# Performance work log

Hardware: AMD Instinct MI355X
Metric: run time of the kernel (lower is better)

The kernel has to match this reference:

```python
import jax, jax.numpy as jnp
import numpy as np

N_NODES = 50000
N_EDGES = 800000
D = 64
N_BASIS = 8


def setup_inputs() -> dict:
    key = jax.random.key(0)
    ks = jax.random.split(key, 16)
    inp = {
        "p": jax.random.normal(ks[0], (N_NODES, D), dtype=jnp.float32),
        "idx_i": jax.random.randint(ks[1], (N_EDGES,), 0, N_NODES),
        "idx_j": jax.random.randint(ks[2], (N_EDGES,), 0, N_NODES),
        "basis": jax.random.normal(ks[3], (N_EDGES, N_BASIS), dtype=jnp.float32),
        # pp_layer MLP: [64, 64, 64], activation tanh between layers
        "pp_W1": jax.random.normal(ks[4], (D, D), dtype=jnp.float32) / np.sqrt(D),
        "pp_b1": jnp.zeros((D,), dtype=jnp.float32),
        "pp_W2": jax.random.normal(ks[5], (D, D), dtype=jnp.float32) / np.sqrt(D),
        "pp_b2": jnp.zeros((D,), dtype=jnp.float32),
        # pi_layer MLP: n_neurons = [128, 64, 64, 64*8], activation=None, last layer no bias
        "pi_W1": jax.random.normal(ks[6], (2 * D, D), dtype=jnp.float32) / np.sqrt(2 * D),
        "pi_b1": jnp.zeros((D,), dtype=jnp.float32),
        "pi_W2": jax.random.normal(ks[7], (D, D), dtype=jnp.float32) / np.sqrt(D),
        "pi_b2": jnp.zeros((D,), dtype=jnp.float32),
        "pi_W3": jax.random.normal(ks[8], (D, D * N_BASIS), dtype=jnp.float32) / np.sqrt(D),
        # ii_layer MLP: [64, 64, 64], activation tanh between layers
        "ii_W1": jax.random.normal(ks[9], (D, D), dtype=jnp.float32) / np.sqrt(D),
        "ii_b1": jnp.zeros((D,), dtype=jnp.float32),
        "ii_W2": jax.random.normal(ks[10], (D, D), dtype=jnp.float32) / np.sqrt(D),
        "ii_b2": jnp.zeros((D,), dtype=jnp.float32),
    }
    return inp


def reference(p, idx_i, idx_j, basis,
              pp_W1, pp_b1, pp_W2, pp_b2,
              pi_W1, pi_b1, pi_W2, pi_b2, pi_W3,
              ii_W1, ii_b1, ii_W2, ii_b2):
    # pp_layer: node MLP (tanh between layers, no activation after last)
    p1 = jnp.tanh(p @ pp_W1 + pp_b1) @ pp_W2 + pp_b2          # [N, D]

    # PILayer: gather endpoint features, concat, linear MLP (activation=None), basis contraction
    inter = jnp.concatenate([p1[idx_i], p1[idx_j]], axis=-1)  # [E, 2D]
    inter = inter @ pi_W1 + pi_b1                              # [E, D]
    inter = inter @ pi_W2 + pi_b2                              # [E, D]
    inter = inter @ pi_W3                                      # [E, D*n_basis] (no bias)
    inter = inter.reshape(inter.shape[0], D, N_BASIS)          # [E, D, n_basis]
    i1 = jnp.einsum('ecb,eb->ec', inter, basis)                # [E, D]

    # ii_layer: edge MLP
    i1 = jnp.tanh(i1 @ ii_W1 + ii_b1) @ ii_W2 + ii_b2          # [E, D]

    # IPLayer: scatter_add edge features back to nodes (dim_size = p1.shape[0])
    out = jax.ops.segment_sum(i1, idx_j, num_segments=p1.shape[0])  # [N, D]
    return out
```

## Files before the change

kernel.cpp:

```cpp
#include <hip/hip_runtime.h>

#define N_NODES 50000
#define N_EDGES 800000

typedef float f32x4 __attribute__((ext_vector_type(4)));
typedef short bf16x8 __attribute__((ext_vector_type(8)));

__device__ __forceinline__ float fast_tanh(float x) {
  float e = __expf(2.0f * x);
  return 1.0f - 2.0f / (e + 1.0f);
}

__device__ __forceinline__ unsigned short f2bf_rne(float x) {
  unsigned u = __float_as_uint(x);
  unsigned r = u + 0x7FFFu + ((u >> 16) & 1u);
  return (unsigned short)(r >> 16);
}

__global__ __launch_bounds__(256) void prep1_kernel(
    const float* __restrict__ piW1, const float* __restrict__ pib1,
    const float* __restrict__ piW2, const float* __restrict__ pib2,
    float* __restrict__ W12, float* __restrict__ b12) {
  int gid = blockIdx.x * 256 + threadIdx.x;
  if (gid < 128 * 64) {
    int m = gid >> 6, c = gid & 63;
    float acc = 0.f;
    #pragma unroll 8
    for (int k = 0; k < 64; ++k) acc = fmaf(piW1[m * 64 + k], piW2[k * 64 + c], acc);
    W12[gid] = acc;
  } else if (gid < 128 * 64 + 64) {
    int c = gid - 128 * 64;
    float acc = pib2[c];
    for (int k = 0; k < 64; ++k) acc = fmaf(pib1[k], piW2[k * 64 + c], acc);
    b12[c] = acc;
  }
}

__global__ __launch_bounds__(256) void prep_b_kernel(
    const float* __restrict__ piW3, const float* __restrict__ iiW1,
    unsigned short* __restrict__ Bpack) {
  int gid = blockIdx.x * 256 + threadIdx.x;
  int j = gid & 7;
  int lane = (gid >> 3) & 63;
  int ct = (gid >> 9) & 3;
  int ks = gid >> 11;
  int kidx = ks * 32 + ((lane >> 4) << 3) + j;
  int col = ct * 16 + (lane & 15);
  int k = kidx >> 3, b = kidx & 7;
  float acc = 0.f;
  #pragma unroll 8
  for (int mm = 0; mm < 64; ++mm)
    acc = fmaf(piW3[k * 512 + mm * 8 + b], iiW1[mm * 64 + col], acc);
  Bpack[gid] = f2bf_rne(acc);
}

__global__ __launch_bounds__(256) void prep_w2_kernel(
    const float* __restrict__ iiW2, unsigned short* __restrict__ W2pack) {
  int gid = blockIdx.x * 256 + threadIdx.x;
  int j = gid & 7;
  int lane = (gid >> 3) & 63;
  int ct = (gid >> 9) & 3;
  int ks = gid >> 11;
  int kidx = ks * 32 + ((lane >> 4) << 3) + j;
  int col = ct * 16 + (lane & 15);
  W2pack[gid] = f2bf_rne(iiW2[kidx * 64 + col]);
}

__global__ __launch_bounds__(256) void node_kernel(
    const float* __restrict__ p,
    const float* __restrict__ ppW1, const float* __restrict__ ppb1,
    const float* __restrict__ ppW2, const float* __restrict__ ppb2,
    const float* __restrict__ W12,
    float* __restrict__ qa, float* __restrict__ qb) {
  __shared__ float sW1[64 * 64];
  __shared__ float sW2[64 * 64];
  __shared__ float sW12[128 * 64];
  __shared__ float sb1[64], sb2[64];
  __shared__ float sX[4][8][64];
  int tid = threadIdx.x;
  for (int i = tid; i < 64 * 64; i += 256) { sW1[i] = ppW1[i]; sW2[i] = ppW2[i]; }
  for (int i = tid; i < 128 * 64; i += 256) sW12[i] = W12[i];
  if (tid < 64) { sb1[tid] = ppb1[tid]; sb2[tid] = ppb2[tid]; }
  __syncthreads();
  int wave = tid >> 6, lane = tid & 63;
  int rowbase = blockIdx.x * 32 + wave * 8;

  float4* sXf4 = (float4*)&sX[wave][0][0];
  for (int t = lane; t < 128; t += 64) {
    int r = t >> 4, c4 = t & 15;
    int row = rowbase + r;
    float4 v = make_float4(0.f, 0.f, 0.f, 0.f);
    if (row < N_NODES) v = ((const float4*)p)[row * 16 + c4];
    sXf4[t] = v;
  }
  __syncthreads();

  float h[8];
  #pragma unroll
  for (int r = 0; r < 8; ++r) h[r] = sb1[lane];
  for (int k = 0; k < 64; ++k) {
    float w = sW1[k * 64 + lane];
    #pragma unroll
    for (int r = 0; r < 8; ++r) h[r] = fmaf(sX[wave][r][k], w, h[r]);
  }
  #pragma unroll
  for (int r = 0; r < 8; ++r) h[r] = fast_tanh(h[r]);
  __syncthreads();
  #pragma unroll
  for (int r = 0; r < 8; ++r) sX[wave][r][lane] = h[r];
  __syncthreads();

  float g[8];
  #pragma unroll
  for (int r = 0; r < 8; ++r) g[r] = sb2[lane];
  for (int k = 0; k < 64; ++k) {
    float w = sW2[k * 64 + lane];
    #pragma unroll
    for (int r = 0; r < 8; ++r) g[r] = fmaf(sX[wave][r][k], w, g[r]);
  }
  __syncthreads();
  #pragma unroll
  for (int r = 0; r < 8; ++r) sX[wave][r][lane] = g[r];
  __syncthreads();

  float a[8], b[8];
  #pragma unroll
  for (int r = 0; r < 8; ++r) { a[r] = 0.f; b[r] = 0.f; }
  for (int k = 0; k < 64; ++k) {
    float wa = sW12[k * 64 + lane];
    float wb = sW12[(64 + k) * 64 + lane];
    #pragma unroll
    for (int r = 0; r < 8; ++r) {
      float x = sX[wave][r][k];
      a[r] = fmaf(x, wa, a[r]);
      b[r] = fmaf(x, wb, b[r]);
    }
  }
  #pragma unroll
  for (int r = 0; r < 8; ++r) {
    int row = rowbase + r;
    if (row < N_NODES) {
      qa[row * 64 + lane] = a[r];
      qb[row * 64 + lane] = b[r];
    }
  }
}

__global__ __launch_bounds__(512, 4) void edge_kernel(
    const int* __restrict__ idx_i, const int* __restrict__ idx_j,
    const float* __restrict__ basis,
    const float* __restrict__ qa, const float* __restrict__ qb,
    const float* __restrict__ b12,
    const unsigned short* __restrict__ Bpack,
    const unsigned short* __restrict__ W2pack,
    const float* __restrict__ iib1, const float* __restrict__ iib2,
    float* __restrict__ out) {
  __shared__ __align__(16) unsigned short sB[32768];
  float* sH2 = (float*)sB;
  unsigned short* sT = sB;

  int tid = threadIdx.x;
  int e0 = blockIdx.x * 128;

  for (int t = tid; t < 2048; t += 512) {
    int e = t >> 4, q = t & 15;
    int ii = idx_i[e0 + e];
    int jj = idx_j[e0 + e];
    float4 va = ((const float4*)qa)[ii * 16 + q];
    float4 vb = ((const float4*)qb)[jj * 16 + q];
    float4 vc = ((const float4*)b12)[q];
    float4 h;
    h.x = va.x + vb.x + vc.x;
    h.y = va.y + vb.y + vc.y;
    h.z = va.z + vb.z + vc.z;
    h.w = va.w + vb.w + vc.w;
    ((float4*)(sH2 + e * 68))[q] = h;
  }
  __syncthreads();

  int w = tid >> 6, l = tid & 63;
  int m = l & 15, s = l >> 4;
  int eloc = w * 16 + m;

  float h2r[16];
  #pragma unroll
  for (int t = 0; t < 16; ++t) h2r[t] = sH2[eloc * 68 + t * 4 + s];

  float bas[8];
  {
    const float4* bp = (const float4*)(basis + (size_t)(e0 + eloc) * 8);
    float4 b0 = bp[0], b1 = bp[1];
    bas[0] = b0.x; bas[1] = b0.y; bas[2] = b0.z; bas[3] = b0.w;
    bas[4] = b1.x; bas[5] = b1.y; bas[6] = b1.z; bas[7] = b1.w;
  }
  __syncthreads();

  {
    const uint4* g = (const uint4*)Bpack;
    uint4* d = (uint4*)sB;
    #pragma unroll
    for (int t = 0; t < 8; ++t) d[tid + t * 512] = g[tid + t * 512];
  }
  __syncthreads();

  f32x4 c0, c1, c2, c3;
  {
    float v0 = iib1[m], v1 = iib1[16 + m], v2 = iib1[32 + m], v3 = iib1[48 + m];
    c0 = (f32x4){v0, v0, v0, v0};
    c1 = (f32x4){v1, v1, v1, v1};
    c2 = (f32x4){v2, v2, v2, v2};
    c3 = (f32x4){v3, v3, v3, v3};
  }

  const bf16x8* Bl = (const bf16x8*)sB;
  #pragma unroll
  for (int ks = 0; ks < 16; ++ks) {
    bf16x8 B0 = Bl[(ks * 4 + 0) * 64 + l];
    bf16x8 B1 = Bl[(ks * 4 + 1) * 64 + l];
    bf16x8 B2 = Bl[(ks * 4 + 2) * 64 + l];
    bf16x8 B3 = Bl[(ks * 4 + 3) * 64 + l];
    float hv = h2r[ks];
    union { unsigned u[4]; bf16x8 v; } Ah, Al;
    #pragma unroll
    for (int jj2 = 0; jj2 < 4; ++jj2) {
      float p0 = hv * bas[2 * jj2];
      float p1 = hv * bas[2 * jj2 + 1];
      unsigned u0 = __float_as_uint(p0), u1 = __float_as_uint(p1);
      unsigned h0 = u0 & 0xFFFF0000u, h1 = u1 & 0xFFFF0000u;
      Ah.u[jj2] = (u0 >> 16) | h1;
      float l0 = p0 - __uint_as_float(h0);
      float l1 = p1 - __uint_as_float(h1);
      Al.u[jj2] = (__float_as_uint(l0) >> 16) | (__float_as_uint(l1) & 0xFFFF0000u);
    }
    c0 = __builtin_amdgcn_mfma_f32_16x16x32_bf16(Ah.v, B0, c0, 0, 0, 0);
    c1 = __builtin_amdgcn_mfma_f32_16x16x32_bf16(Ah.v, B1, c1, 0, 0, 0);
    c2 = __builtin_amdgcn_mfma_f32_16x16x32_bf16(Ah.v, B2, c2, 0, 0, 0);
    c3 = __builtin_amdgcn_mfma_f32_16x16x32_bf16(Ah.v, B3, c3, 0, 0, 0);
    c0 = __builtin_amdgcn_mfma_f32_16x16x32_bf16(Al.v, B0, c0, 0, 0, 0);
    c1 = __builtin_amdgcn_mfma_f32_16x16x32_bf16(Al.v, B1, c1, 0, 0, 0);
    c2 = __builtin_amdgcn_mfma_f32_16x16x32_bf16(Al.v, B2, c2, 0, 0, 0);
    c3 = __builtin_amdgcn_mfma_f32_16x16x32_bf16(Al.v, B3, c3, 0, 0, 0);
  }
  __syncthreads();

  #pragma unroll
  for (int r = 0; r < 4; ++r) {
    int row = w * 16 + s * 4 + r;
    sT[row * 72 + 0 * 16 + m] = f2bf_rne(fast_tanh(c0[r]));
    sT[row * 72 + 1 * 16 + m] = f2bf_rne(fast_tanh(c1[r]));
    sT[row * 72 + 2 * 16 + m] = f2bf_rne(fast_tanh(c2[r]));
    sT[row * 72 + 3 * 16 + m] = f2bf_rne(fast_tanh(c3[r]));
  }
  __syncthreads();

  f32x4 d0, d1, d2, d3;
  {
    float v0 = iib2[m], v1 = iib2[16 + m], v2 = iib2[32 + m], v3 = iib2[48 + m];
    d0 = (f32x4){v0, v0, v0, v0};
    d1 = (f32x4){v1, v1, v1, v1};
    d2 = (f32x4){v2, v2, v2, v2};
    d3 = (f32x4){v3, v3, v3, v3};
  }
  const bf16x8* Wl = (const bf16x8*)W2pack;
  #pragma unroll
  for (int ks = 0; ks < 2; ++ks) {
    bf16x8 Af = *(const bf16x8*)(sT + eloc * 72 + ks * 32 + s * 8);
    d0 = __builtin_amdgcn_mfma_f32_16x16x32_bf16(Af, Wl[(ks * 4 + 0) * 64 + l], d0, 0, 0, 0);
    d1 = __builtin_amdgcn_mfma_f32_16x16x32_bf16(Af, Wl[(ks * 4 + 1) * 64 + l], d1, 0, 0, 0);
    d2 = __builtin_amdgcn_mfma_f32_16x16x32_bf16(Af, Wl[(ks * 4 + 2) * 64 + l], d2, 0, 0, 0);
    d3 = __builtin_amdgcn_mfma_f32_16x16x32_bf16(Af, Wl[(ks * 4 + 3) * 64 + l], d3, 0, 0, 0);
  }

  #pragma unroll
  for (int r = 0; r < 4; ++r) {
    int jj = idx_j[e0 + w * 16 + s * 4 + r];
    float* po = out + (size_t)jj * 64;
    atomicAdd(po + m, d0[r]);
    atomicAdd(po + 16 + m, d1[r]);
    atomicAdd(po + 32 + m, d2[r]);
    atomicAdd(po + 48 + m, d3[r]);
  }
}

extern "C" void kernel_launch(void* const* d_in, const int* in_sizes, int n_in,
                              void* d_out, int out_size, void* d_ws, size_t ws_size,
                              hipStream_t stream) {
  const float* p     = (const float*)d_in[0];
  const int*   idx_i = (const int*)d_in[1];
  const int*   idx_j = (const int*)d_in[2];
  const float* basis = (const float*)d_in[3];
  const float* ppW1  = (const float*)d_in[4];
  const float* ppb1  = (const float*)d_in[5];
  const float* ppW2  = (const float*)d_in[6];
  const float* ppb2  = (const float*)d_in[7];
  const float* piW1  = (const float*)d_in[8];
  const float* pib1  = (const float*)d_in[9];
  const float* piW2  = (const float*)d_in[10];
  const float* pib2  = (const float*)d_in[11];
  const float* piW3  = (const float*)d_in[12];
  const float* iiW1  = (const float*)d_in[13];
  const float* iib1  = (const float*)d_in[14];
  const float* iiW2  = (const float*)d_in[15];
  const float* iib2  = (const float*)d_in[16];

  float* ws  = (float*)d_ws;
  float* qa  = ws;
  float* qb  = ws + 3200000;
  float* W12 = ws + 6400000;
  float* b12 = ws + 6408192;
  unsigned short* Bpack  = (unsigned short*)(ws + 6408256);
  unsigned short* W2pack = (unsigned short*)(ws + 6408256 + 16384);

  hipMemsetAsync(d_out, 0, (size_t)out_size * sizeof(float), stream);
  prep1_kernel<<<33, 256, 0, stream>>>(piW1, pib1, piW2, pib2, W12, b12);
  prep_b_kernel<<<128, 256, 0, stream>>>(piW3, iiW1, Bpack);
  prep_w2_kernel<<<16, 256, 0, stream>>>(iiW2, W2pack);
  node_kernel<<<1563, 256, 0, stream>>>(p, ppW1, ppb1, ppW2, ppb2, W12, qa, qb);
  edge_kernel<<<6250, 512, 0, stream>>>(idx_i, idx_j, basis, qa, qb, b12,
                                        Bpack, W2pack, iib1, iib2, (float*)d_out);
}
```

Before: 291.1 us.

## Use single-bf16 MFMA, 1024-thread edge blocks, and XOR-swizzled LDS staging

The edge kernel drops the hi/lo split-bf16 emulation of fp32 and converts the basis-scaled products once with v_cvt_pk_bf16_f32. This halves the first-stage MFMA count and removes the bit-manipulation ALU work, at the cost of accuracy in that contraction. Blocks now process 256 edges with 1024 threads, so the 64KB weight pack is loaded into LDS half as often per edge. The padded stride-68 staging buffer is replaced by an XOR-swizzled stride-64 layout so 256 edges fit in the same LDS. The new launch bounds may tighten the register budget and risk spills.

```diff
diff --git a/kernel.cpp b/kernel.cpp
--- a/kernel.cpp
+++ b/kernel.cpp
@@ -146,7 +146,7 @@
   }
 }
 
-__global__ __launch_bounds__(512, 4) void edge_kernel(
+__global__ __launch_bounds__(1024, 8) void edge_kernel(
     const int* __restrict__ idx_i, const int* __restrict__ idx_j,
     const float* __restrict__ basis,
     const float* __restrict__ qa, const float* __restrict__ qb,
@@ -160,9 +160,9 @@
   unsigned short* sT = sB;
 
   int tid = threadIdx.x;
-  int e0 = blockIdx.x * 128;
-
-  for (int t = tid; t < 2048; t += 512) {
+  int e0 = blockIdx.x * 256;
+
+  for (int t = tid; t < 4096; t += 1024) {
     int e = t >> 4, q = t & 15;
     int ii = idx_i[e0 + e];
     int jj = idx_j[e0 + e];
@@ -174,17 +174,19 @@
     h.y = va.y + vb.y + vc.y;
     h.z = va.z + vb.z + vc.z;
     h.w = va.w + vb.w + vc.w;
-    ((float4*)(sH2 + e * 68))[q] = h;
+    int dw = e * 64 + ((q * 4) ^ ((e & 7) << 3));
+    *((float4*)(sH2 + dw)) = h;
   }
   __syncthreads();
 
   int w = tid >> 6, l = tid & 63;
   int m = l & 15, s = l >> 4;
   int eloc = w * 16 + m;
+  int swz = (eloc & 7) << 3;
 
   float h2r[16];
   #pragma unroll
-  for (int t = 0; t < 16; ++t) h2r[t] = sH2[eloc * 68 + t * 4 + s];
+  for (int t = 0; t < 16; ++t) h2r[t] = sH2[eloc * 64 + ((t * 4 + s) ^ swz)];
 
   float bas[8];
   {
@@ -199,7 +201,7 @@
     const uint4* g = (const uint4*)Bpack;
     uint4* d = (uint4*)sB;
     #pragma unroll
-    for (int t = 0; t < 8; ++t) d[tid + t * 512] = g[tid + t * 512];
+    for (int t = 0; t < 4; ++t) d[tid + t * 1024] = g[tid + t * 1024];
   }
   __syncthreads();
 
@@ -220,26 +222,17 @@
     bf16x8 B2 = Bl[(ks * 4 + 2) * 64 + l];
     bf16x8 B3 = Bl[(ks * 4 + 3) * 64 + l];
     float hv = h2r[ks];
-    union { unsigned u[4]; bf16x8 v; } Ah, Al;
-    #pragma unroll
-    for (int jj2 = 0; jj2 < 4; ++jj2) {
-      float p0 = hv * bas[2 * jj2];
-      float p1 = hv * bas[2 * jj2 + 1];
-      unsigned u0 = __float_as_uint(p0), u1 = __float_as_uint(p1);
-      unsigned h0 = u0 & 0xFFFF0000u, h1 = u1 & 0xFFFF0000u;
-      Ah.u[jj2] = (u0 >> 16) | h1;
-      float l0 = p0 - __uint_as_float(h0);
-      float l1 = p1 - __uint_as_float(h1);
-      Al.u[jj2] = (__float_as_uint(l0) >> 16) | (__float_as_uint(l1) & 0xFFFF0000u);
+    union { unsigned u[4]; bf16x8 v; } A;
+    #pragma unroll
+    for (int j = 0; j < 4; ++j) {
+      float p0 = hv * bas[2 * j];
+      float p1 = hv * bas[2 * j + 1];
+      asm("v_cvt_pk_bf16_f32 %0, %1, %2" : "=v"(A.u[j]) : "v"(p0), "v"(p1));
     }
-    c0 = __builtin_amdgcn_mfma_f32_16x16x32_bf16(Ah.v, B0, c0, 0, 0, 0);
-    c1 = __builtin_amdgcn_mfma_f32_16x16x32_bf16(Ah.v, B1, c1, 0, 0, 0);
-    c2 = __builtin_amdgcn_mfma_f32_16x16x32_bf16(Ah.v, B2, c2, 0, 0, 0);
-    c3 = __builtin_amdgcn_mfma_f32_16x16x32_bf16(Ah.v, B3, c3, 0, 0, 0);
-    c0 = __builtin_amdgcn_mfma_f32_16x16x32_bf16(Al.v, B0, c0, 0, 0, 0);
-    c1 = __builtin_amdgcn_mfma_f32_16x16x32_bf16(Al.v, B1, c1, 0, 0, 0);
-    c2 = __builtin_amdgcn_mfma_f32_16x16x32_bf16(Al.v, B2, c2, 0, 0, 0);
-    c3 = __builtin_amdgcn_mfma_f32_16x16x32_bf16(Al.v, B3, c3, 0, 0, 0);
+    c0 = __builtin_amdgcn_mfma_f32_16x16x32_bf16(A.v, B0, c0, 0, 0, 0);
+    c1 = __builtin_amdgcn_mfma_f32_16x16x32_bf16(A.v, B1, c1, 0, 0, 0);
+    c2 = __builtin_amdgcn_mfma_f32_16x16x32_bf16(A.v, B2, c2, 0, 0, 0);
+    c3 = __builtin_amdgcn_mfma_f32_16x16x32_bf16(A.v, B3, c3, 0, 0, 0);
   }
   __syncthreads();
 
@@ -316,6 +309,6 @@
   prep_b_kernel<<<128, 256, 0, stream>>>(piW3, iiW1, Bpack);
   prep_w2_kernel<<<16, 256, 0, stream>>>(iiW2, W2pack);
   node_kernel<<<1563, 256, 0, stream>>>(p, ppW1, ppb1, ppW2, ppb2, W12, qa, qb);
-  edge_kernel<<<6250, 512, 0, stream>>>(idx_i, idx_j, basis, qa, qb, b12,
-                                        Bpack, W2pack, iib1, iib2, (float*)d_out);
-}
+  edge_kernel<<<3125, 1024, 0, stream>>>(idx_i, idx_j, basis, qa, qb, b12,
+                                         Bpack, W2pack, iib1, iib2, (float*)d_out);
+}
```

New measurement: 300.5 us. +3.2%, slower.
